# Kernel tuning notes

Measured on AMD Instinct MI355X. Metric: run time of the kernel, lower is better.

## Reference

```python
import jax, jax.numpy as jnp
import numpy as np

TEMPERATURE = 4.0

def setup_inputs() -> dict:
    key = jax.random.key(0)
    k1, k2 = jax.random.split(key)
    query = jax.random.normal(k1, (128, 128, 256), dtype=jnp.float32)      # (B, D, Q)
    context = jax.random.normal(k2, (128, 128, 32, 32), dtype=jnp.float32)  # (B, D, H, W)
    return {"query": query, "context": context}

def reference(query, context):
    B, D, Q = query.shape
    H, W = context.shape[2], context.shape[3]
    L = H * W  # context_length
    context_flat = context.reshape(B, D, L)                    # (B, D, L)
    # scores[b, l, q] = sum_d context[b, d, l] * query[b, d, q]
    scores = jnp.einsum('bdl,bdq->blq', context_flat, query)   # (B, L, Q)
    # first softmax: over query dim (context -> query)
    attn_q = jax.nn.softmax(scores, axis=-1)                   # (B, L, Q)
    # second softmax: over context dim with temperature (query -> context)
    attn_c = jax.nn.softmax(attn_q.transpose(0, 2, 1) * TEMPERATURE, axis=-1)  # (B, Q, L)
    # weighted_context[b, d, q] = sum_l context[b, d, l] * attn_c[b, q, l]
    weighted_context = jnp.einsum('bdl,bql->bdq', context_flat, attn_c)  # (B, D, Q)
    attention_map = attn_c.reshape(B, Q, H, W)
    return (weighted_context, attention_map)
```

## Files before the change

### kernel.cpp

```cpp
#include <hip/hip_runtime.h>
#include <math.h>

#define B_ 128
#define D_ 128
#define Q_ 256
#define L_ 1024

typedef __attribute__((ext_vector_type(8))) short s16x8;
typedef __attribute__((ext_vector_type(4))) float f32x4;

__device__ __forceinline__ unsigned short f2bf(float x) {
  unsigned u = __float_as_uint(x);
  u += 0x7FFF + ((u >> 16) & 1);
  return (unsigned short)(u >> 16);
}
__device__ __forceinline__ float bf2f(unsigned short h) {
  return __uint_as_float(((unsigned)h) << 16);
}
__device__ __forceinline__ uint2 pack4bf(float4 v) {
  uint2 r;
  r.x = ((unsigned)f2bf(v.y) << 16) | (unsigned)f2bf(v.x);
  r.y = ((unsigned)f2bf(v.w) << 16) | (unsigned)f2bf(v.z);
  return r;
}
__device__ __forceinline__ void split8(const float* x, s16x8& hi, s16x8& lo) {
#pragma unroll
  for (int j = 0; j < 8; j++) {
    unsigned short h = f2bf(x[j]);
    hi[j] = (short)h;
    lo[j] = (short)f2bf(x[j] - bf2f(h));
  }
}

__global__ __launch_bounds__(256, 2) void k1_attnq(
    const float* __restrict__ query, const float* __restrict__ ctx,
    float* __restrict__ attq, float* __restrict__ pd) {
  __shared__ float sm[4][64], ss[4][64], fm[64], fs[64];
  const int lt = blockIdx.x, b = blockIdx.y;
  const int l0 = lt * 64;
  const int tid = threadIdx.x;
  const int wq = tid >> 6;
  const int lane = tid & 63, quad = lane >> 4, l15 = lane & 15;

  const float* Qb = query + (size_t)b * D_ * Q_;
  const float* Cb = ctx + (size_t)b * D_ * L_ + l0;

  f32x4 acc[4][4];
#pragma unroll
  for (int mi = 0; mi < 4; mi++)
#pragma unroll
    for (int ni = 0; ni < 4; ni++) acc[mi][ni] = (f32x4){0.f, 0.f, 0.f, 0.f};

#pragma unroll 2
  for (int k0 = 0; k0 < D_; k0 += 32) {
    const int kq = k0 + quad * 8;
    s16x8 ah[4], al[4], bh[4], bl[4];
#pragma unroll
    for (int mi = 0; mi < 4; mi++) {
      const float* p = Qb + (size_t)kq * Q_ + wq * 64 + mi * 16 + l15;
      float x[8];
#pragma unroll
      for (int j = 0; j < 8; j++) x[j] = p[(size_t)j * Q_];
      split8(x, ah[mi], al[mi]);
    }
#pragma unroll
    for (int ni = 0; ni < 4; ni++) {
      const float* p = Cb + (size_t)kq * L_ + ni * 16 + l15;
      float x[8];
#pragma unroll
      for (int j = 0; j < 8; j++) x[j] = p[(size_t)j * L_];
      split8(x, bh[ni], bl[ni]);
    }
#pragma unroll
    for (int mi = 0; mi < 4; mi++)
#pragma unroll
      for (int ni = 0; ni < 4; ni++) {
        acc[mi][ni] = __builtin_amdgcn_mfma_f32_16x16x32_bf16(
            ah[mi], bh[ni], acc[mi][ni], 0, 0, 0);
        acc[mi][ni] = __builtin_amdgcn_mfma_f32_16x16x32_bf16(
            ah[mi], bl[ni], acc[mi][ni], 0, 0, 0);
        acc[mi][ni] = __builtin_amdgcn_mfma_f32_16x16x32_bf16(
            al[mi], bh[ni], acc[mi][ni], 0, 0, 0);
      }
  }

#pragma unroll
  for (int ni = 0; ni < 4; ni++) {
    float m = -1e30f;
#pragma unroll
    for (int mi = 0; mi < 4; mi++)
#pragma unroll
      for (int r = 0; r < 4; r++) m = fmaxf(m, acc[mi][ni][r]);
    m = fmaxf(m, __shfl_xor(m, 16));
    m = fmaxf(m, __shfl_xor(m, 32));
    float s = 0.f;
#pragma unroll
    for (int mi = 0; mi < 4; mi++)
#pragma unroll
      for (int r = 0; r < 4; r++) s += __expf(acc[mi][ni][r] - m);
    s += __shfl_xor(s, 16);
    s += __shfl_xor(s, 32);
    if (quad == 0) {
      sm[wq][ni * 16 + l15] = m;
      ss[wq][ni * 16 + l15] = s;
    }
  }
  __syncthreads();
  if (tid < 64) {
    float m0 = sm[0][tid], m1 = sm[1][tid], m2 = sm[2][tid], m3 = sm[3][tid];
    float M = fmaxf(fmaxf(m0, m1), fmaxf(m2, m3));
    float S = ss[0][tid] * __expf(m0 - M) + ss[1][tid] * __expf(m1 - M) +
              ss[2][tid] * __expf(m2 - M) + ss[3][tid] * __expf(m3 - M);
    fm[tid] = M;
    fs[tid] = 1.f / S;
  }
  __syncthreads();

  float fmv[4], fiv[4];
#pragma unroll
  for (int ni = 0; ni < 4; ni++) {
    fmv[ni] = fm[ni * 16 + l15];
    fiv[ni] = fs[ni * 16 + l15];
  }
  float* Ab = attq + ((size_t)b * Q_ + wq * 64) * L_ + l0;
  float dsum[4][4];
#pragma unroll
  for (int mi = 0; mi < 4; mi++)
#pragma unroll
    for (int r = 0; r < 4; r++) dsum[mi][r] = 0.f;
#pragma unroll
  for (int mi = 0; mi < 4; mi++)
#pragma unroll
    for (int r = 0; r < 4; r++) {
      const int q = mi * 16 + quad * 4 + r;
#pragma unroll
      for (int ni = 0; ni < 4; ni++) {
        float a = __expf(acc[mi][ni][r] - fmv[ni]) * fiv[ni];
        Ab[(size_t)q * L_ + ni * 16 + l15] = a;
        dsum[mi][r] += __expf(4.f * a);
      }
    }
#pragma unroll
  for (int mi = 0; mi < 4; mi++)
#pragma unroll
    for (int r = 0; r < 4; r++) {
      float v = dsum[mi][r];
      v += __shfl_xor(v, 1);
      v += __shfl_xor(v, 2);
      v += __shfl_xor(v, 4);
      v += __shfl_xor(v, 8);
      dsum[mi][r] = v;
    }
  if (l15 == 0) {
#pragma unroll
    for (int mi = 0; mi < 4; mi++)
#pragma unroll
      for (int r = 0; r < 4; r++)
        pd[(size_t)lt * (B_ * Q_) + b * Q_ + wq * 64 + mi * 16 + quad * 4 +
           r] = dsum[mi][r];
  }
}

__global__ __launch_bounds__(256) void k2_invd(const float* __restrict__ pd,
                                               float* __restrict__ invd) {
  const int i = blockIdx.x * 256 + threadIdx.x;
  float s = 0.f;
#pragma unroll
  for (int t = 0; t < 16; t++) s += pd[(size_t)t * (B_ * Q_) + i];
  invd[i] = 1.f / s;
}

__global__ __launch_bounds__(256) void k4_weighted(
    const float* __restrict__ ctx, float* __restrict__ attn,
    const float* __restrict__ invd, float* __restrict__ W) {
  __shared__ unsigned short As[128][32];
  __shared__ unsigned short Bs[64][32];
  const int b = blockIdx.y, q0 = blockIdx.x * 64;
  const int tid = threadIdx.x;
  const int w = tid >> 6, lane = tid & 63, quad = lane >> 4, l15 = lane & 15;
  const int wd = (w >> 1) * 64, wn = (w & 1) * 32;

  const float* Cb = ctx + (size_t)b * D_ * L_;
  float* Ab = attn + ((size_t)b * Q_ + q0) * L_;

  const int lc = (tid & 7) * 4;
  const int rr = tid >> 3;
  const float id0 = invd[b * Q_ + q0 + rr];
  const float id1 = invd[b * Q_ + q0 + rr + 32];

  f32x4 acc[4][2];
#pragma unroll
  for (int mi = 0; mi < 4; mi++)
#pragma unroll
    for (int ni = 0; ni < 2; ni++) acc[mi][ni] = (f32x4){0.f, 0.f, 0.f, 0.f};

  for (int l0 = 0; l0 < L_; l0 += 32) {
    if (l0) __syncthreads();
#pragma unroll
    for (int h = 0; h < 4; h++) {
      const int d = rr + h * 32;
      float4 cv = *(const float4*)(Cb + (size_t)d * L_ + l0 + lc);
      *(uint2*)&As[d][lc] = pack4bf(cv);
    }
#pragma unroll
    for (int h = 0; h < 2; h++) {
      const int q = rr + h * 32;
      float* p = Ab + (size_t)q * L_ + l0 + lc;
      float4 a = *(const float4*)p;
      const float idv = h ? id1 : id0;
      float4 t;
      t.x = __expf(4.f * a.x) * idv;
      t.y = __expf(4.f * a.y) * idv;
      t.z = __expf(4.f * a.z) * idv;
      t.w = __expf(4.f * a.w) * idv;
      *(float4*)p = t;
      *(uint2*)&Bs[q][lc] = pack4bf(t);
    }
    __syncthreads();

    s16x8 af[4], bq[2];
#pragma unroll
    for (int mi = 0; mi < 4; mi++)
      af[mi] = *(const s16x8*)&As[wd + mi * 16 + l15][quad * 8];
#pragma unroll
    for (int ni = 0; ni < 2; ni++)
      bq[ni] = *(const s16x8*)&Bs[wn + ni * 16 + l15][quad * 8];
#pragma unroll
    for (int mi = 0; mi < 4; mi++)
#pragma unroll
      for (int ni = 0; ni < 2; ni++)
        acc[mi][ni] = __builtin_amdgcn_mfma_f32_16x16x32_bf16(
            af[mi], bq[ni], acc[mi][ni], 0, 0, 0);
  }

  float* Wb = W + (size_t)b * D_ * Q_;
#pragma unroll
  for (int mi = 0; mi < 4; mi++)
#pragma unroll
    for (int ni = 0; ni < 2; ni++)
#pragma unroll
      for (int r = 0; r < 4; r++)
        Wb[(size_t)(wd + mi * 16 + quad * 4 + r) * Q_ + q0 + wn + ni * 16 +
           l15] = acc[mi][ni][r];
}

extern "C" void kernel_launch(void* const* d_in, const int* in_sizes, int n_in,
                              void* d_out, int out_size, void* d_ws,
                              size_t ws_size, hipStream_t stream) {
  const float* query = (const float*)d_in[0];
  const float* ctx = (const float*)d_in[1];
  float* W = (float*)d_out;
  float* attn = (float*)d_out + (size_t)B_ * D_ * Q_;

  const size_t need = (size_t)17 * B_ * Q_ * sizeof(float);
  float* pd = (ws_size >= need && d_ws) ? (float*)d_ws : W;
  float* invd = pd + (size_t)16 * B_ * Q_;

  k1_attnq<<<dim3(L_ / 64, B_), 256, 0, stream>>>(query, ctx, attn, pd);
  k2_invd<<<dim3(B_ * Q_ / 256), 256, 0, stream>>>(pd, invd);
  k4_weighted<<<dim3(Q_ / 64, B_), 256, 0, stream>>>(ctx, attn, invd, W);
}
```

Baseline: 316.2 us.

## Pre-split query into bf16 hi/lo transposed buffers and stage context via LDS

Adds a pre-pass kernel that transposes the query and splits it into bf16 hi/lo halves in a workspace, laid out so each MFMA fragment is a contiguous 16-byte load. The score kernel now reads these pre-split fragments and stages the context tile through swizzled shared memory, converting it once per block instead of per wave with strided scalar loads. The goal is to remove the redundant strided global reads and repeated hi/lo splitting in the first kernel. In exchange it adds an extra launch, extra workspace traffic and block-level syncs, and it raises the occupancy hint to 3. The old path is kept as a fallback when the workspace is too small.

```diff
diff --git a/kernel.cpp b/kernel.cpp
--- a/kernel.cpp
+++ b/kernel.cpp
@@ -8,13 +8,14 @@
 
 typedef __attribute__((ext_vector_type(8))) short s16x8;
 typedef __attribute__((ext_vector_type(4))) float f32x4;
-
-__device__ __forceinline__ unsigned short f2bf(float x) {
+typedef unsigned short u16;
+
+__device__ __forceinline__ u16 f2bf(float x) {
   unsigned u = __float_as_uint(x);
   u += 0x7FFF + ((u >> 16) & 1);
-  return (unsigned short)(u >> 16);
-}
-__device__ __forceinline__ float bf2f(unsigned short h) {
+  return (u16)(u >> 16);
+}
+__device__ __forceinline__ float bf2f(u16 h) {
   return __uint_as_float(((unsigned)h) << 16);
 }
 __device__ __forceinline__ uint2 pack4bf(float4 v) {
@@ -26,13 +27,197 @@
 __device__ __forceinline__ void split8(const float* x, s16x8& hi, s16x8& lo) {
 #pragma unroll
   for (int j = 0; j < 8; j++) {
-    unsigned short h = f2bf(x[j]);
+    u16 h = f2bf(x[j]);
     hi[j] = (short)h;
     lo[j] = (short)f2bf(x[j] - bf2f(h));
   }
 }
 
-__global__ __launch_bounds__(256, 2) void k1_attnq(
+__global__ __launch_bounds__(256) void k0_split(const float* __restrict__ query,
+                                                u16* __restrict__ qhi,
+                                                u16* __restrict__ qlo) {
+  __shared__ float sm0[128][65];
+  const int b = blockIdx.y, q0 = blockIdx.x * 64;
+  const int tid = threadIdx.x;
+  {
+    const int dr = tid >> 4;
+    const int lc = (tid & 15) * 4;
+#pragma unroll
+    for (int h = 0; h < 8; h++) {
+      const int d = h * 16 + dr;
+      float4 v = *(const float4*)(query + ((size_t)b * D_ + d) * Q_ + q0 + lc);
+      sm0[d][lc] = v.x;
+      sm0[d][lc + 1] = v.y;
+      sm0[d][lc + 2] = v.z;
+      sm0[d][lc + 3] = v.w;
+    }
+  }
+  __syncthreads();
+  const int qr = tid >> 2;
+  const int dc = (tid & 3) * 32;
+  u16* ph = qhi + ((size_t)b * Q_ + q0 + qr) * D_ + dc;
+  u16* pl = qlo + ((size_t)b * Q_ + q0 + qr) * D_ + dc;
+#pragma unroll
+  for (int c = 0; c < 4; c++) {
+    s16x8 hv, lv;
+#pragma unroll
+    for (int j = 0; j < 8; j++) {
+      float x = sm0[dc + c * 8 + j][qr];
+      u16 h = f2bf(x);
+      hv[j] = (short)h;
+      lv[j] = (short)f2bf(x - bf2f(h));
+    }
+    *(s16x8*)(ph + c * 8) = hv;
+    *(s16x8*)(pl + c * 8) = lv;
+  }
+}
+
+__global__ __launch_bounds__(256, 3) void k1_attnq(
+    const u16* __restrict__ qhi, const u16* __restrict__ qlo,
+    const float* __restrict__ ctx, float* __restrict__ attq,
+    float* __restrict__ pd) {
+  __shared__ u16 CsH[64][48], CsL[64][48];
+  __shared__ float sm[4][64], ss[4][64], fm[64], fs[64];
+  const int lt = blockIdx.x, b = blockIdx.y;
+  const int l0 = lt * 64;
+  const int tid = threadIdx.x;
+  const int wq = tid >> 6;
+  const int lane = tid & 63, quad = lane >> 4, l15 = lane & 15;
+
+  const float* Cb = ctx + (size_t)b * D_ * L_ + l0;
+  const u16* Qh = qhi + ((size_t)b * Q_ + wq * 64 + l15) * D_;
+  const u16* Ql = qlo + ((size_t)b * Q_ + wq * 64 + l15) * D_;
+
+  const int dd = tid >> 3;
+  const int lc = (tid & 7) * 8;
+
+  f32x4 acc[4][4];
+#pragma unroll
+  for (int mi = 0; mi < 4; mi++)
+#pragma unroll
+    for (int ni = 0; ni < 4; ni++) acc[mi][ni] = (f32x4){0.f, 0.f, 0.f, 0.f};
+
+#pragma unroll 2
+  for (int k0 = 0; k0 < D_; k0 += 32) {
+    if (k0) __syncthreads();
+    const float* cp = Cb + (size_t)(k0 + dd) * L_ + lc;
+    float4 v0 = *(const float4*)cp;
+    float4 v1 = *(const float4*)(cp + 4);
+    float xv[8] = {v0.x, v0.y, v0.z, v0.w, v1.x, v1.y, v1.z, v1.w};
+#pragma unroll
+    for (int j = 0; j < 8; j++) {
+      const int ll = lc + j;
+      const int col = ((((dd >> 3) ^ (ll >> 3)) & 3) << 3) | (dd & 7);
+      u16 h = f2bf(xv[j]);
+      CsH[ll][col] = h;
+      CsL[ll][col] = f2bf(xv[j] - bf2f(h));
+    }
+    __syncthreads();
+
+    s16x8 bh[4], bl[4];
+#pragma unroll
+    for (int ni = 0; ni < 4; ni++) {
+      const int ll = ni * 16 + l15;
+      const int cc = ((quad ^ (ll >> 3)) & 3) << 3;
+      bh[ni] = *(const s16x8*)&CsH[ll][cc];
+      bl[ni] = *(const s16x8*)&CsL[ll][cc];
+    }
+#pragma unroll
+    for (int mi = 0; mi < 4; mi++) {
+      const s16x8 ah =
+          *(const s16x8*)(Qh + (size_t)mi * 16 * D_ + k0 + quad * 8);
+      const s16x8 al =
+          *(const s16x8*)(Ql + (size_t)mi * 16 * D_ + k0 + quad * 8);
+#pragma unroll
+      for (int ni = 0; ni < 4; ni++) {
+        acc[mi][ni] = __builtin_amdgcn_mfma_f32_16x16x32_bf16(
+            ah, bh[ni], acc[mi][ni], 0, 0, 0);
+        acc[mi][ni] = __builtin_amdgcn_mfma_f32_16x16x32_bf16(
+            ah, bl[ni], acc[mi][ni], 0, 0, 0);
+        acc[mi][ni] = __builtin_amdgcn_mfma_f32_16x16x32_bf16(
+            al, bh[ni], acc[mi][ni], 0, 0, 0);
+      }
+    }
+  }
+
+#pragma unroll
+  for (int ni = 0; ni < 4; ni++) {
+    float m = -1e30f;
+#pragma unroll
+    for (int mi = 0; mi < 4; mi++)
+#pragma unroll
+      for (int r = 0; r < 4; r++) m = fmaxf(m, acc[mi][ni][r]);
+    m = fmaxf(m, __shfl_xor(m, 16));
+    m = fmaxf(m, __shfl_xor(m, 32));
+    float s = 0.f;
+#pragma unroll
+    for (int mi = 0; mi < 4; mi++)
+#pragma unroll
+      for (int r = 0; r < 4; r++) s += __expf(acc[mi][ni][r] - m);
+    s += __shfl_xor(s, 16);
+    s += __shfl_xor(s, 32);
+    if (quad == 0) {
+      sm[wq][ni * 16 + l15] = m;
+      ss[wq][ni * 16 + l15] = s;
+    }
+  }
+  __syncthreads();
+  if (tid < 64) {
+    float m0 = sm[0][tid], m1 = sm[1][tid], m2 = sm[2][tid], m3 = sm[3][tid];
+    float M = fmaxf(fmaxf(m0, m1), fmaxf(m2, m3));
+    float S = ss[0][tid] * __expf(m0 - M) + ss[1][tid] * __expf(m1 - M) +
+              ss[2][tid] * __expf(m2 - M) + ss[3][tid] * __expf(m3 - M);
+    fm[tid] = M;
+    fs[tid] = 1.f / S;
+  }
+  __syncthreads();
+
+  float fmv[4], fiv[4];
+#pragma unroll
+  for (int ni = 0; ni < 4; ni++) {
+    fmv[ni] = fm[ni * 16 + l15];
+    fiv[ni] = fs[ni * 16 + l15];
+  }
+  float* Ab = attq + ((size_t)b * Q_ + wq * 64) * L_ + l0;
+  float dsum[4][4];
+#pragma unroll
+  for (int mi = 0; mi < 4; mi++)
+#pragma unroll
+    for (int r = 0; r < 4; r++) dsum[mi][r] = 0.f;
+#pragma unroll
+  for (int mi = 0; mi < 4; mi++)
+#pragma unroll
+    for (int r = 0; r < 4; r++) {
+      const int q = mi * 16 + quad * 4 + r;
+#pragma unroll
+      for (int ni = 0; ni < 4; ni++) {
+        float a = __expf(acc[mi][ni][r] - fmv[ni]) * fiv[ni];
+        Ab[(size_t)q * L_ + ni * 16 + l15] = a;
+        dsum[mi][r] += __expf(4.f * a);
+      }
+    }
+#pragma unroll
+  for (int mi = 0; mi < 4; mi++)
+#pragma unroll
+    for (int r = 0; r < 4; r++) {
+      float v = dsum[mi][r];
+      v += __shfl_xor(v, 1);
+      v += __shfl_xor(v, 2);
+      v += __shfl_xor(v, 4);
+      v += __shfl_xor(v, 8);
+      dsum[mi][r] = v;
+    }
+  if (l15 == 0) {
+#pragma unroll
+    for (int mi = 0; mi < 4; mi++)
+#pragma unroll
+      for (int r = 0; r < 4; r++)
+        pd[(size_t)lt * (B_ * Q_) + b * Q_ + wq * 64 + mi * 16 + quad * 4 +
+           r] = dsum[mi][r];
+  }
+}
+
+__global__ __launch_bounds__(256, 2) void k1_attnq_legacy(
     const float* __restrict__ query, const float* __restrict__ ctx,
     float* __restrict__ attq, float* __restrict__ pd) {
   __shared__ float sm[4][64], ss[4][64], fm[64], fs[64];
@@ -252,11 +437,25 @@
   float* W = (float*)d_out;
   float* attn = (float*)d_out + (size_t)B_ * D_ * Q_;
 
-  const size_t need = (size_t)17 * B_ * Q_ * sizeof(float);
-  float* pd = (ws_size >= need && d_ws) ? (float*)d_ws : W;
-  float* invd = pd + (size_t)16 * B_ * Q_;
-
-  k1_attnq<<<dim3(L_ / 64, B_), 256, 0, stream>>>(query, ctx, attn, pd);
-  k2_invd<<<dim3(B_ * Q_ / 256), 256, 0, stream>>>(pd, invd);
-  k4_weighted<<<dim3(Q_ / 64, B_), 256, 0, stream>>>(ctx, attn, invd, W);
-}
+  const size_t nQT = (size_t)B_ * Q_ * D_;
+  const size_t need_pd = (size_t)17 * B_ * Q_ * sizeof(float);
+  const size_t need_full = nQT * 2 * sizeof(u16) + need_pd;
+
+  if (d_ws && ws_size >= need_full) {
+    u16* qh = (u16*)d_ws;
+    u16* ql = qh + nQT;
+    float* pd = (float*)(ql + nQT);
+    float* invd = pd + (size_t)16 * B_ * Q_;
+    k0_split<<<dim3(Q_ / 64, B_), 256, 0, stream>>>(query, qh, ql);
+    k1_attnq<<<dim3(L_ / 64, B_), 256, 0, stream>>>(qh, ql, ctx, attn, pd);
+    k2_invd<<<dim3(B_ * Q_ / 256), 256, 0, stream>>>(pd, invd);
+    k4_weighted<<<dim3(Q_ / 64, B_), 256, 0, stream>>>(ctx, attn, invd, W);
+  } else {
+    float* pd = (d_ws && ws_size >= need_pd) ? (float*)d_ws : W;
+    float* invd = pd + (size_t)16 * B_ * Q_;
+    k1_attnq_legacy<<<dim3(L_ / 64, B_), 256, 0, stream>>>(query, ctx, attn,
+                                                           pd);
+    k2_invd<<<dim3(B_ * Q_ / 256), 256, 0, stream>>>(pd, invd);
+    k4_weighted<<<dim3(Q_ / 64, B_), 256, 0, stream>>>(ctx, attn, invd, W);
+  }
+}
```

Result: slower. 332.9 us (+5.3%).

## Stage attention tile in LDS for coalesced stores and fold invd into weighted kernel

Applied to the files above, without the earlier changes.

In the first kernel, softmax outputs are written into a padded shared-memory tile and then stored to global memory as row-contiguous float4 writes, replacing scattered 4-byte stores. The separate kernel that reduced partial denominators is removed, and that reduction now runs at the start of the weighted-context kernel. This saves a launch and a round-trip through global memory. In exchange, k1 uses about 70KB more LDS, which may lower occupancy below the two blocks per CU its launch bounds request, and every k4 block repeats a small reduction.

```diff
diff --git a/kernel.cpp b/kernel.cpp
--- a/kernel.cpp
+++ b/kernel.cpp
@@ -8,13 +8,14 @@
 
 typedef __attribute__((ext_vector_type(8))) short s16x8;
 typedef __attribute__((ext_vector_type(4))) float f32x4;
-
-__device__ __forceinline__ unsigned short f2bf(float x) {
+typedef unsigned short u16;
+
+__device__ __forceinline__ u16 f2bf(float x) {
   unsigned u = __float_as_uint(x);
   u += 0x7FFF + ((u >> 16) & 1);
-  return (unsigned short)(u >> 16);
-}
-__device__ __forceinline__ float bf2f(unsigned short h) {
+  return (u16)(u >> 16);
+}
+__device__ __forceinline__ float bf2f(u16 h) {
   return __uint_as_float(((unsigned)h) << 16);
 }
 __device__ __forceinline__ uint2 pack4bf(float4 v) {
@@ -26,7 +27,7 @@
 __device__ __forceinline__ void split8(const float* x, s16x8& hi, s16x8& lo) {
 #pragma unroll
   for (int j = 0; j < 8; j++) {
-    unsigned short h = f2bf(x[j]);
+    u16 h = f2bf(x[j]);
     hi[j] = (short)h;
     lo[j] = (short)f2bf(x[j] - bf2f(h));
   }
@@ -35,6 +36,7 @@
 __global__ __launch_bounds__(256, 2) void k1_attnq(
     const float* __restrict__ query, const float* __restrict__ ctx,
     float* __restrict__ attq, float* __restrict__ pd) {
+  __shared__ float att[4][64][68];
   __shared__ float sm[4][64], ss[4][64], fm[64], fs[64];
   const int lt = blockIdx.x, b = blockIdx.y;
   const int l0 = lt * 64;
@@ -128,18 +130,26 @@
   for (int mi = 0; mi < 4; mi++)
 #pragma unroll
     for (int r = 0; r < 4; r++) dsum[mi][r] = 0.f;
+
 #pragma unroll
   for (int mi = 0; mi < 4; mi++)
 #pragma unroll
     for (int r = 0; r < 4; r++) {
-      const int q = mi * 16 + quad * 4 + r;
+      const int ql = mi * 16 + quad * 4 + r;
 #pragma unroll
       for (int ni = 0; ni < 4; ni++) {
         float a = __expf(acc[mi][ni][r] - fmv[ni]) * fiv[ni];
-        Ab[(size_t)q * L_ + ni * 16 + l15] = a;
+        att[wq][ql][ni * 16 + l15] = a;
         dsum[mi][r] += __expf(4.f * a);
       }
     }
+#pragma unroll
+  for (int g = 0; g < 16; g++) {
+    const int ql = g * 4 + quad;
+    float4 v = *(const float4*)&att[wq][ql][l15 * 4];
+    *(float4*)(Ab + (size_t)ql * L_ + l15 * 4) = v;
+  }
+
 #pragma unroll
   for (int mi = 0; mi < 4; mi++)
 #pragma unroll
@@ -161,32 +171,33 @@
   }
 }
 
-__global__ __launch_bounds__(256) void k2_invd(const float* __restrict__ pd,
-                                               float* __restrict__ invd) {
-  const int i = blockIdx.x * 256 + threadIdx.x;
-  float s = 0.f;
-#pragma unroll
-  for (int t = 0; t < 16; t++) s += pd[(size_t)t * (B_ * Q_) + i];
-  invd[i] = 1.f / s;
-}
-
 __global__ __launch_bounds__(256) void k4_weighted(
     const float* __restrict__ ctx, float* __restrict__ attn,
-    const float* __restrict__ invd, float* __restrict__ W) {
+    const float* __restrict__ pd, float* __restrict__ W) {
   __shared__ unsigned short As[128][32];
   __shared__ unsigned short Bs[64][32];
+  __shared__ float ivs[64];
   const int b = blockIdx.y, q0 = blockIdx.x * 64;
   const int tid = threadIdx.x;
   const int w = tid >> 6, lane = tid & 63, quad = lane >> 4, l15 = lane & 15;
   const int wd = (w >> 1) * 64, wn = (w & 1) * 32;
 
+  if (tid < 64) {
+    float s = 0.f;
+#pragma unroll
+    for (int t = 0; t < 16; t++)
+      s += pd[(size_t)t * (B_ * Q_) + b * Q_ + q0 + tid];
+    ivs[tid] = 1.f / s;
+  }
+  __syncthreads();
+
   const float* Cb = ctx + (size_t)b * D_ * L_;
   float* Ab = attn + ((size_t)b * Q_ + q0) * L_;
 
   const int lc = (tid & 7) * 4;
   const int rr = tid >> 3;
-  const float id0 = invd[b * Q_ + q0 + rr];
-  const float id1 = invd[b * Q_ + q0 + rr + 32];
+  const float id0 = ivs[rr];
+  const float id1 = ivs[rr + 32];
 
   f32x4 acc[4][2];
 #pragma unroll
@@ -252,11 +263,9 @@
   float* W = (float*)d_out;
   float* attn = (float*)d_out + (size_t)B_ * D_ * Q_;
 
-  const size_t need = (size_t)17 * B_ * Q_ * sizeof(float);
-  float* pd = (ws_size >= need && d_ws) ? (float*)d_ws : W;
-  float* invd = pd + (size_t)16 * B_ * Q_;
+  const size_t need_pd = (size_t)16 * B_ * Q_ * sizeof(float);
+  float* pd = (d_ws && ws_size >= need_pd) ? (float*)d_ws : W;
 
   k1_attnq<<<dim3(L_ / 64, B_), 256, 0, stream>>>(query, ctx, attn, pd);
-  k2_invd<<<dim3(B_ * Q_ / 256), 256, 0, stream>>>(pd, invd);
-  k4_weighted<<<dim3(Q_ / 64, B_), 256, 0, stream>>>(ctx, attn, invd, W);
-}
+  k4_weighted<<<dim3(Q_ / 64, B_), 256, 0, stream>>>(ctx, attn, pd, W);
+}
```

Result: slower. 351.4 us (+11.1%).
